# Kernel tuning notes

Measured on AMD Instinct MI355X. Metric: run time of the kernel, lower is better.

The kernel has to match this reference:

```python
import jax, jax.numpy as jnp
import numpy as np

N = 100000
E = 2000000
IN_DIM = 5
D = 32
L = 3
EPS = 1e-5


def setup_inputs() -> dict:
    key = jax.random.key(0)
    ks = jax.random.split(key, 10)
    x = jax.random.normal(ks[0], (N, IN_DIM), dtype=jnp.float32)
    edge_index = jax.random.randint(ks[1], (2, E), 0, N, dtype=jnp.int64)
    s = 1.0 / np.sqrt(D)
    w_in = jax.random.normal(ks[2], (D, IN_DIM), dtype=jnp.float32) / np.sqrt(IN_DIM)
    b_in = jnp.zeros((D,), dtype=jnp.float32)
    w_l = jax.random.normal(ks[3], (L, D, D), dtype=jnp.float32) * s  # lin_l per layer
    b_l = jnp.zeros((L, D), dtype=jnp.float32)
    w_r = jax.random.normal(ks[4], (L, D, D), dtype=jnp.float32) * s  # lin_r per layer (no bias, as in PyG SAGEConv)
    gamma = jnp.ones((D,), dtype=jnp.float32)
    beta = jnp.zeros((D,), dtype=jnp.float32)
    return {"x": x, "edge_index": edge_index, "w_in": w_in, "b_in": b_in,
            "w_l": w_l, "b_l": b_l, "w_r": w_r, "gamma": gamma, "beta": beta}


def _layernorm(h, gamma, beta):
    mu = jnp.mean(h, axis=-1, keepdims=True)
    var = jnp.mean(jnp.square(h - mu), axis=-1, keepdims=True)
    return (h - mu) * jax.lax.rsqrt(var + EPS) * gamma + beta


def reference(x, edge_index, w_in, b_in, w_l, b_l, w_r, gamma, beta):
    src = edge_index[0]
    dst = edge_index[1]
    n = x.shape[0]
    # node in-degree for mean aggregation (0-degree nodes get 0 output, like scatter_mean)
    deg = jax.ops.segment_sum(jnp.ones((src.shape[0],), dtype=x.dtype), dst, num_segments=n)
    inv_deg = (1.0 / jnp.maximum(deg, 1.0))[:, None]  # [N,1]
    h = x @ w_in.T + b_in  # [N, D]
    for i in range(w_l.shape[0]):
        msg = h[src]  # [E, D] gather
        agg = jax.ops.segment_sum(msg, dst, num_segments=n) * inv_deg  # mean aggregate
        h = agg @ w_l[i].T + b_l[i] + h @ w_r[i].T  # SAGEConv: lin_l(aggr) + lin_r(x)
        h = _layernorm(jax.nn.relu(h), gamma, beta)
    return h
```

## Files before the change

### kernel.cpp

```cpp
#include <hip/hip_runtime.h>
#include <hip/hip_bf16.h>

#define DIM 32
#define INDIM 5
#define EPB 4096
#define BKBITS 7
#define BKN 128
#define NBMAX 1024
#define CAP 4096

__device__ __forceinline__ unsigned short f2bf(float f) {
    unsigned u = __float_as_uint(f);
    u += 0x7FFFu + ((u >> 16) & 1u);
    return (unsigned short)(u >> 16);
}
__device__ __forceinline__ float bf2f_lo(unsigned u) { return __uint_as_float(u << 16); }
__device__ __forceinline__ float bf2f_hi(unsigned u) { return __uint_as_float(u & 0xFFFF0000u); }


__global__ __launch_bounds__(256) void bucket_count_kernel(const int* __restrict__ dst,
                                                           int* __restrict__ bcnt, int e, int nb) {
    __shared__ int hist[NBMAX];
    int t = threadIdx.x;
    for (int i = t; i < nb; i += 256) hist[i] = 0;
    __syncthreads();
    int base = blockIdx.x * EPB;
    for (int k = 0; k < EPB; k += 256) {
        int i = base + k + t;
        if (i < e) atomicAdd(&hist[dst[i] >> BKBITS], 1);
    }
    __syncthreads();
    for (int i = t; i < nb; i += 256) {
        int h = hist[i];
        if (h) atomicAdd(&bcnt[i], h);
    }
}


__global__ void bucket_scan_kernel(const int* __restrict__ bcnt, int* __restrict__ bbase,
                                   int* __restrict__ bcur, int* __restrict__ row_ptr,
                                   int nb, int n, int e) {
    __shared__ int s[1024];
    int t = threadIdx.x;
    int v = (t < nb) ? bcnt[t] : 0;
    s[t] = v;
    __syncthreads();
    for (int o = 1; o < 1024; o <<= 1) {
        int a = (t >= o) ? s[t - o] : 0;
        __syncthreads();
        s[t] += a;
        __syncthreads();
    }
    if (t < nb) {
        int excl = s[t] - v;
        bbase[t] = excl;
        bcur[t] = excl;
    }
    if (t == 0) {
        bbase[nb] = e;
        row_ptr[n] = e;
    }
}


__global__ __launch_bounds__(256) void bucket_fill_kernel(const int* __restrict__ src,
                                                          const int* __restrict__ dst,
                                                          int* __restrict__ bcur,
                                                          unsigned* __restrict__ packed,
                                                          int e, int nb) {
    __shared__ unsigned sw[EPB];
    __shared__ unsigned short sb[EPB];
    __shared__ int hist[NBMAX];
    __shared__ int rbase[NBMAX];
    int t = threadIdx.x;
    for (int i = t; i < nb; i += 256) hist[i] = 0;
    __syncthreads();
    int base = blockIdx.x * EPB;
    for (int k = 0; k < EPB; k += 256) {
        int i = base + k + t;
        if (i < e) {
            int s = src[i];
            int d = dst[i];
            int b = d >> BKBITS;
            sw[k + t] = ((unsigned)s << BKBITS) | (unsigned)(d & (BKN - 1));
            sb[k + t] = (unsigned short)b;
            atomicAdd(&hist[b], 1);
        }
    }
    __syncthreads();
    for (int i = t; i < nb; i += 256) {
        int h = hist[i];
        rbase[i] = h ? atomicAdd(&bcur[i], h) : 0;
        hist[i] = 0;
    }
    __syncthreads();
    for (int k = 0; k < EPB; k += 256) {
        int i = base + k + t;
        if (i < e) {
            int b = sb[k + t];
            int r = atomicAdd(&hist[b], 1);
            packed[rbase[b] + r] = sw[k + t];
        }
    }
}


__global__ __launch_bounds__(256) void csr_build_kernel(const unsigned* __restrict__ packed,
                                                        const int* __restrict__ bbase,
                                                        int* __restrict__ row_ptr,
                                                        int* __restrict__ esrc, int n) {
    __shared__ unsigned ew[CAP];
    __shared__ int h2[BKN];
    __shared__ int off[BKN];
    int b = blockIdx.x;
    int base = bbase[b];
    int cnt = bbase[b + 1] - base;
    int t = threadIdx.x;
    if (t < BKN) h2[t] = 0;
    __syncthreads();
    bool staged = (cnt <= CAP);
    for (int i = t; i < cnt; i += 256) {
        unsigned w = packed[base + i];
        if (staged) ew[i] = w;
        atomicAdd(&h2[w & (BKN - 1)], 1);
    }
    __syncthreads();
    int v = 0;
    if (t < BKN) {
        v = h2[t];
        off[t] = v;
    }
    __syncthreads();
    for (int o = 1; o < BKN; o <<= 1) {
        int a = 0;
        if (t < BKN && t >= o) a = off[t - o];
        __syncthreads();
        if (t < BKN) off[t] += a;
        __syncthreads();
    }
    if (t < BKN) {
        int excl = off[t] - v;
        __syncthreads();
        off[t] = excl;
        h2[t] = 0;
    } else {
        __syncthreads();
    }
    __syncthreads();
    int node = b * BKN + t;
    if (t < BKN && node < n) row_ptr[node] = base + off[t];
    for (int i = t; i < cnt; i += 256) {
        unsigned w = staged ? ew[i] : packed[base + i];
        int dl = w & (BKN - 1);
        int r = atomicAdd(&h2[dl], 1);
        esrc[base + off[dl] + r] = (int)(w >> BKBITS);
    }
}


__global__ void input_proj_kernel(const float* __restrict__ x, const float* __restrict__ w_in,
                                  const float* __restrict__ b_in,
                                  unsigned short* __restrict__ h, int n) {
    __shared__ float sw[DIM * INDIM];
    __shared__ float sb[DIM];
    int t = threadIdx.x;
    if (t < DIM * INDIM) sw[t] = w_in[t];
    if (t < DIM) sb[t] = b_in[t];
    __syncthreads();
    int idx = blockIdx.x * 256 + t;
    int node = idx >> 5;
    int d = idx & 31;
    if (node < n) {
        const float* xr = x + (size_t)node * INDIM;
        float acc = sb[d];
#pragma unroll
        for (int k = 0; k < INDIM; k++) acc = fmaf(xr[k], sw[d * INDIM + k], acc);
        h[(size_t)node * DIM + d] = f2bf(acc);
    }
}


template <int LAST>
__global__ __launch_bounds__(128, 4) void layer_fused_kernel(
    const int* __restrict__ row_ptr, const int* __restrict__ esrc,
    const unsigned short* __restrict__ h_in,
    unsigned short* __restrict__ h_out_bf, float* __restrict__ out_f32,
    const float* __restrict__ wl, const float* __restrict__ bl,
    const float* __restrict__ wr, const float* __restrict__ gamma,
    const float* __restrict__ beta, int n) {
    __shared__ float sAgg[32][DIM];
    __shared__ float sSelf[32][DIM];

    int t = threadIdx.x;
    int d = t & 31;

    int nd = t >> 2;
    int q = t & 3;
    int node = blockIdx.x * 32 + nd;
    const uint4* hv = (const uint4*)h_in;

    if (node < n) {
        {
            uint4 v = hv[(size_t)node * 4 + q];
            float4 f0 = make_float4(bf2f_lo(v.x), bf2f_hi(v.x), bf2f_lo(v.y), bf2f_hi(v.y));
            float4 f1 = make_float4(bf2f_lo(v.z), bf2f_hi(v.z), bf2f_lo(v.w), bf2f_hi(v.w));
            *(float4*)&sSelf[nd][q * 8] = f0;
            *(float4*)&sSelf[nd][q * 8 + 4] = f1;
        }
        int rs = row_ptr[node];
        int re = row_ptr[node + 1];
        float a0 = 0.f, a1 = 0.f, a2 = 0.f, a3 = 0.f, a4 = 0.f, a5 = 0.f, a6 = 0.f, a7 = 0.f;
        int j = rs;
        int i0, i1, i2, i3, i4, i5, i6, i7;
        bool have = (j + 8 <= re);
        if (have) {
            i0 = esrc[j];     i1 = esrc[j + 1]; i2 = esrc[j + 2]; i3 = esrc[j + 3];
            i4 = esrc[j + 4]; i5 = esrc[j + 5]; i6 = esrc[j + 6]; i7 = esrc[j + 7];
        }
        while (have) {
            int jn = j + 8;
            bool haven = (jn + 8 <= re);
            int t0, t1, t2, t3, t4, t5, t6, t7;
            if (haven) {
                t0 = esrc[jn];     t1 = esrc[jn + 1]; t2 = esrc[jn + 2]; t3 = esrc[jn + 3];
                t4 = esrc[jn + 4]; t5 = esrc[jn + 5]; t6 = esrc[jn + 6]; t7 = esrc[jn + 7];
            }
            uint4 v0 = hv[(size_t)i0 * 4 + q];
            uint4 v1 = hv[(size_t)i1 * 4 + q];
            uint4 v2 = hv[(size_t)i2 * 4 + q];
            uint4 v3 = hv[(size_t)i3 * 4 + q];
            uint4 v4 = hv[(size_t)i4 * 4 + q];
            uint4 v5 = hv[(size_t)i5 * 4 + q];
            uint4 v6 = hv[(size_t)i6 * 4 + q];
            uint4 v7 = hv[(size_t)i7 * 4 + q];
            a0 += bf2f_lo(v0.x); a1 += bf2f_hi(v0.x); a2 += bf2f_lo(v0.y); a3 += bf2f_hi(v0.y);
            a4 += bf2f_lo(v0.z); a5 += bf2f_hi(v0.z); a6 += bf2f_lo(v0.w); a7 += bf2f_hi(v0.w);
            a0 += bf2f_lo(v1.x); a1 += bf2f_hi(v1.x); a2 += bf2f_lo(v1.y); a3 += bf2f_hi(v1.y);
            a4 += bf2f_lo(v1.z); a5 += bf2f_hi(v1.z); a6 += bf2f_lo(v1.w); a7 += bf2f_hi(v1.w);
            a0 += bf2f_lo(v2.x); a1 += bf2f_hi(v2.x); a2 += bf2f_lo(v2.y); a3 += bf2f_hi(v2.y);
            a4 += bf2f_lo(v2.z); a5 += bf2f_hi(v2.z); a6 += bf2f_lo(v2.w); a7 += bf2f_hi(v2.w);
            a0 += bf2f_lo(v3.x); a1 += bf2f_hi(v3.x); a2 += bf2f_lo(v3.y); a3 += bf2f_hi(v3.y);
            a4 += bf2f_lo(v3.z); a5 += bf2f_hi(v3.z); a6 += bf2f_lo(v3.w); a7 += bf2f_hi(v3.w);
            a0 += bf2f_lo(v4.x); a1 += bf2f_hi(v4.x); a2 += bf2f_lo(v4.y); a3 += bf2f_hi(v4.y);
            a4 += bf2f_lo(v4.z); a5 += bf2f_hi(v4.z); a6 += bf2f_lo(v4.w); a7 += bf2f_hi(v4.w);
            a0 += bf2f_lo(v5.x); a1 += bf2f_hi(v5.x); a2 += bf2f_lo(v5.y); a3 += bf2f_hi(v5.y);
            a4 += bf2f_lo(v5.z); a5 += bf2f_hi(v5.z); a6 += bf2f_lo(v5.w); a7 += bf2f_hi(v5.w);
            a0 += bf2f_lo(v6.x); a1 += bf2f_hi(v6.x); a2 += bf2f_lo(v6.y); a3 += bf2f_hi(v6.y);
            a4 += bf2f_lo(v6.z); a5 += bf2f_hi(v6.z); a6 += bf2f_lo(v6.w); a7 += bf2f_hi(v6.w);
            a0 += bf2f_lo(v7.x); a1 += bf2f_hi(v7.x); a2 += bf2f_lo(v7.y); a3 += bf2f_hi(v7.y);
            a4 += bf2f_lo(v7.z); a5 += bf2f_hi(v7.z); a6 += bf2f_lo(v7.w); a7 += bf2f_hi(v7.w);
            j = jn;
            have = haven;
            if (haven) {
                i0 = t0; i1 = t1; i2 = t2; i3 = t3; i4 = t4; i5 = t5; i6 = t6; i7 = t7;
            }
        }
        for (; j < re; ++j) {
            int s = esrc[j];
            uint4 v = hv[(size_t)s * 4 + q];
            a0 += bf2f_lo(v.x); a1 += bf2f_hi(v.x); a2 += bf2f_lo(v.y); a3 += bf2f_hi(v.y);
            a4 += bf2f_lo(v.z); a5 += bf2f_hi(v.z); a6 += bf2f_lo(v.w); a7 += bf2f_hi(v.w);
        }
        float iv = 1.f / fmaxf((float)(re - rs), 1.f);
        float4 f0 = make_float4(a0 * iv, a1 * iv, a2 * iv, a3 * iv);
        float4 f1 = make_float4(a4 * iv, a5 * iv, a6 * iv, a7 * iv);
        *(float4*)&sAgg[nd][q * 8] = f0;
        *(float4*)&sAgg[nd][q * 8 + 4] = f1;
    }
    __syncthreads();

    float wlr[DIM], wrr[DIM];
    {
        const float4* p1 = (const float4*)(wl + (size_t)d * DIM);
        const float4* p2 = (const float4*)(wr + (size_t)d * DIM);
#pragma unroll
        for (int qq = 0; qq < 8; qq++) {
            float4 a = p1[qq];
            wlr[4 * qq] = a.x; wlr[4 * qq + 1] = a.y; wlr[4 * qq + 2] = a.z; wlr[4 * qq + 3] = a.w;
            float4 c = p2[qq];
            wrr[4 * qq] = c.x; wrr[4 * qq + 1] = c.y; wrr[4 * qq + 2] = c.z; wrr[4 * qq + 3] = c.w;
        }
    }
    float bias = bl[d], g = gamma[d], be = beta[d];

#pragma unroll
    for (int it = 0; it < 8; ++it) {
        int ln = it * 4 + (t >> 5);
        int nodec = blockIdx.x * 32 + ln;
        if (nodec < n) {
            float o = bias;
            const float* va = sAgg[ln];
            const float* vs = sSelf[ln];
#pragma unroll
            for (int qq = 0; qq < 8; qq++) {
                float4 a = *(const float4*)&va[qq * 4];
                float4 s = *(const float4*)&vs[qq * 4];
                o = fmaf(a.x, wlr[4 * qq], o);     o = fmaf(s.x, wrr[4 * qq], o);
                o = fmaf(a.y, wlr[4 * qq + 1], o); o = fmaf(s.y, wrr[4 * qq + 1], o);
                o = fmaf(a.z, wlr[4 * qq + 2], o); o = fmaf(s.z, wrr[4 * qq + 2], o);
                o = fmaf(a.w, wlr[4 * qq + 3], o); o = fmaf(s.w, wrr[4 * qq + 3], o);
            }
            float out = fmaxf(o, 0.f);
            float sum = out, sq = out * out;
#pragma unroll
            for (int off = 16; off > 0; off >>= 1) {
                sum += __shfl_xor(sum, off, 32);
                sq += __shfl_xor(sq, off, 32);
            }
            float mu = sum * (1.f / 32.f);
            float var = fmaxf(sq * (1.f / 32.f) - mu * mu, 0.f);
            float r = rsqrtf(var + 1e-5f);
            float res = (out - mu) * r * g + be;
            if (LAST) out_f32[(size_t)nodec * DIM + d] = res;
            else      h_out_bf[(size_t)nodec * DIM + d] = f2bf(res);
        }
    }
}


extern "C" void kernel_launch(void* const* d_in, const int* in_sizes, int n_in,
                              void* d_out, int out_size, void* d_ws, size_t ws_size,
                              hipStream_t stream) {
    const float* x = (const float*)d_in[0];
    const int* ei = (const int*)d_in[1];
    const float* w_in = (const float*)d_in[2];
    const float* b_in = (const float*)d_in[3];
    const float* w_l = (const float*)d_in[4];
    const float* b_l = (const float*)d_in[5];
    const float* w_r = (const float*)d_in[6];
    const float* gamma = (const float*)d_in[7];
    const float* beta = (const float*)d_in[8];

    int n = in_sizes[0] / INDIM;
    int e = in_sizes[1] / 2;
    int L = in_sizes[4] / (DIM * DIM);
    const int* src = ei;
    const int* dst = ei + e;
    int nb = (n + BKN - 1) >> BKBITS;

    char* w = (char*)d_ws;
    int* bcnt = (int*)w;               w += (size_t)NBMAX * 4;
    int* bbase = (int*)w;              w += (size_t)(NBMAX + 1) * 4;
    int* bcur = (int*)w;               w += (size_t)NBMAX * 4;
    int* row_ptr = (int*)w;            w += (size_t)(n + 1) * 4;
    int* esrc = (int*)w;               w += (size_t)e * 4;
    unsigned short* h_A = (unsigned short*)w;  w += (size_t)n * DIM * 2;
    unsigned short* h_B = (unsigned short*)w;  w += (size_t)n * DIM * 2;
    unsigned* packed = (unsigned*)h_A;

    int nbE = (e + EPB - 1) / EPB;

    hipMemsetAsync(bcnt, 0, (size_t)nb * 4, stream);
    bucket_count_kernel<<<nbE, 256, 0, stream>>>(dst, bcnt, e, nb);
    bucket_scan_kernel<<<1, 1024, 0, stream>>>(bcnt, bbase, bcur, row_ptr, nb, n, e);
    bucket_fill_kernel<<<nbE, 256, 0, stream>>>(src, dst, bcur, packed, e, nb);
    csr_build_kernel<<<nb, 256, 0, stream>>>(packed, bbase, row_ptr, esrc, n);

    input_proj_kernel<<<(n * DIM + 255) / 256, 256, 0, stream>>>(x, w_in, b_in, h_A, n);

    unsigned short* bufs[2] = {h_A, h_B};
    int nbF = (n + 31) / 32;
    for (int i = 0; i < L; i++) {
        const unsigned short* hin = bufs[i & 1];
        unsigned short* hout = bufs[(i + 1) & 1];
        const float* wl = w_l + (size_t)i * DIM * DIM;
        const float* bl = b_l + (size_t)i * DIM;
        const float* wr = w_r + (size_t)i * DIM * DIM;
        if (i == L - 1)
            layer_fused_kernel<1><<<nbF, 128, 0, stream>>>(row_ptr, esrc, hin, nullptr,
                                                           (float*)d_out, wl, bl, wr,
                                                           gamma, beta, n);
        else
            layer_fused_kernel<0><<<nbF, 128, 0, stream>>>(row_ptr, esrc, hin, hout,
                                                           nullptr, wl, bl, wr,
                                                           gamma, beta, n);
    }
}
```

Measured before the change: 242.2 us.

## Split bf16 node features into two half-planes and gather each plane separately

Stores the intermediate bf16 node features as two planes of 16 dims each (planar by half) instead of interleaved 32-dim rows. The aggregation now runs two passes, each gathering 32-byte half-rows, so each plane (3.2 MB) is more likely to stay resident in cache during its gather. The cost is walking each node's edge list twice and issuing narrower loads. It also adds nontemporal loads in the CSR build kernels and removes a redundant barrier.

```diff
diff --git a/kernel.cpp b/kernel.cpp
--- a/kernel.cpp
+++ b/kernel.cpp
@@ -27,7 +27,10 @@
     int base = blockIdx.x * EPB;
     for (int k = 0; k < EPB; k += 256) {
         int i = base + k + t;
-        if (i < e) atomicAdd(&hist[dst[i] >> BKBITS], 1);
+        if (i < e) {
+            int dv = __builtin_nontemporal_load(&dst[i]);
+            atomicAdd(&hist[dv >> BKBITS], 1);
+        }
     }
     __syncthreads();
     for (int i = t; i < nb; i += 256) {
@@ -79,8 +82,8 @@
     for (int k = 0; k < EPB; k += 256) {
         int i = base + k + t;
         if (i < e) {
-            int s = src[i];
-            int d = dst[i];
+            int s = __builtin_nontemporal_load(&src[i]);
+            int d = __builtin_nontemporal_load(&dst[i]);
             int b = d >> BKBITS;
             sw[k + t] = ((unsigned)s << BKBITS) | (unsigned)(d & (BKN - 1));
             sb[k + t] = (unsigned short)b;
@@ -120,7 +123,7 @@
     __syncthreads();
     bool staged = (cnt <= CAP);
     for (int i = t; i < cnt; i += 256) {
-        unsigned w = packed[base + i];
+        unsigned w = __builtin_nontemporal_load(&packed[base + i]);
         if (staged) ew[i] = w;
         atomicAdd(&h2[w & (BKN - 1)], 1);
     }
@@ -140,11 +143,8 @@
     }
     if (t < BKN) {
         int excl = off[t] - v;
-        __syncthreads();
         off[t] = excl;
         h2[t] = 0;
-    } else {
-        __syncthreads();
     }
     __syncthreads();
     int node = b * BKN + t;
@@ -175,7 +175,7 @@
         float acc = sb[d];
 #pragma unroll
         for (int k = 0; k < INDIM; k++) acc = fmaf(xr[k], sw[d * INDIM + k], acc);
-        h[(size_t)node * DIM + d] = f2bf(acc);
+        h[(size_t)(d >> 4) * n * 16 + (size_t)node * 16 + (d & 15)] = f2bf(acc);
     }
 }
 
@@ -193,79 +193,72 @@
 
     int t = threadIdx.x;
     int d = t & 31;
-
     int nd = t >> 2;
     int q = t & 3;
     int node = blockIdx.x * 32 + nd;
-    const uint4* hv = (const uint4*)h_in;
-
+
+    int rs = 0, re = 0;
     if (node < n) {
-        {
-            uint4 v = hv[(size_t)node * 4 + q];
-            float4 f0 = make_float4(bf2f_lo(v.x), bf2f_hi(v.x), bf2f_lo(v.y), bf2f_hi(v.y));
-            float4 f1 = make_float4(bf2f_lo(v.z), bf2f_hi(v.z), bf2f_lo(v.w), bf2f_hi(v.w));
-            *(float4*)&sSelf[nd][q * 8] = f0;
-            *(float4*)&sSelf[nd][q * 8 + 4] = f1;
-        }
-        int rs = row_ptr[node];
-        int re = row_ptr[node + 1];
-        float a0 = 0.f, a1 = 0.f, a2 = 0.f, a3 = 0.f, a4 = 0.f, a5 = 0.f, a6 = 0.f, a7 = 0.f;
-        int j = rs;
-        int i0, i1, i2, i3, i4, i5, i6, i7;
-        bool have = (j + 8 <= re);
-        if (have) {
-            i0 = esrc[j];     i1 = esrc[j + 1]; i2 = esrc[j + 2]; i3 = esrc[j + 3];
-            i4 = esrc[j + 4]; i5 = esrc[j + 5]; i6 = esrc[j + 6]; i7 = esrc[j + 7];
-        }
-        while (have) {
-            int jn = j + 8;
-            bool haven = (jn + 8 <= re);
-            int t0, t1, t2, t3, t4, t5, t6, t7;
-            if (haven) {
-                t0 = esrc[jn];     t1 = esrc[jn + 1]; t2 = esrc[jn + 2]; t3 = esrc[jn + 3];
-                t4 = esrc[jn + 4]; t5 = esrc[jn + 5]; t6 = esrc[jn + 6]; t7 = esrc[jn + 7];
-            }
-            uint4 v0 = hv[(size_t)i0 * 4 + q];
-            uint4 v1 = hv[(size_t)i1 * 4 + q];
-            uint4 v2 = hv[(size_t)i2 * 4 + q];
-            uint4 v3 = hv[(size_t)i3 * 4 + q];
-            uint4 v4 = hv[(size_t)i4 * 4 + q];
-            uint4 v5 = hv[(size_t)i5 * 4 + q];
-            uint4 v6 = hv[(size_t)i6 * 4 + q];
-            uint4 v7 = hv[(size_t)i7 * 4 + q];
-            a0 += bf2f_lo(v0.x); a1 += bf2f_hi(v0.x); a2 += bf2f_lo(v0.y); a3 += bf2f_hi(v0.y);
-            a4 += bf2f_lo(v0.z); a5 += bf2f_hi(v0.z); a6 += bf2f_lo(v0.w); a7 += bf2f_hi(v0.w);
-            a0 += bf2f_lo(v1.x); a1 += bf2f_hi(v1.x); a2 += bf2f_lo(v1.y); a3 += bf2f_hi(v1.y);
-            a4 += bf2f_lo(v1.z); a5 += bf2f_hi(v1.z); a6 += bf2f_lo(v1.w); a7 += bf2f_hi(v1.w);
-            a0 += bf2f_lo(v2.x); a1 += bf2f_hi(v2.x); a2 += bf2f_lo(v2.y); a3 += bf2f_hi(v2.y);
-            a4 += bf2f_lo(v2.z); a5 += bf2f_hi(v2.z); a6 += bf2f_lo(v2.w); a7 += bf2f_hi(v2.w);
-            a0 += bf2f_lo(v3.x); a1 += bf2f_hi(v3.x); a2 += bf2f_lo(v3.y); a3 += bf2f_hi(v3.y);
-            a4 += bf2f_lo(v3.z); a5 += bf2f_hi(v3.z); a6 += bf2f_lo(v3.w); a7 += bf2f_hi(v3.w);
-            a0 += bf2f_lo(v4.x); a1 += bf2f_hi(v4.x); a2 += bf2f_lo(v4.y); a3 += bf2f_hi(v4.y);
-            a4 += bf2f_lo(v4.z); a5 += bf2f_hi(v4.z); a6 += bf2f_lo(v4.w); a7 += bf2f_hi(v4.w);
-            a0 += bf2f_lo(v5.x); a1 += bf2f_hi(v5.x); a2 += bf2f_lo(v5.y); a3 += bf2f_hi(v5.y);
-            a4 += bf2f_lo(v5.z); a5 += bf2f_hi(v5.z); a6 += bf2f_lo(v5.w); a7 += bf2f_hi(v5.w);
-            a0 += bf2f_lo(v6.x); a1 += bf2f_hi(v6.x); a2 += bf2f_lo(v6.y); a3 += bf2f_hi(v6.y);
-            a4 += bf2f_lo(v6.z); a5 += bf2f_hi(v6.z); a6 += bf2f_lo(v6.w); a7 += bf2f_hi(v6.w);
-            a0 += bf2f_lo(v7.x); a1 += bf2f_hi(v7.x); a2 += bf2f_lo(v7.y); a3 += bf2f_hi(v7.y);
-            a4 += bf2f_lo(v7.z); a5 += bf2f_hi(v7.z); a6 += bf2f_lo(v7.w); a7 += bf2f_hi(v7.w);
-            j = jn;
-            have = haven;
-            if (haven) {
-                i0 = t0; i1 = t1; i2 = t2; i3 = t3; i4 = t4; i5 = t5; i6 = t6; i7 = t7;
-            }
-        }
-        for (; j < re; ++j) {
-            int s = esrc[j];
-            uint4 v = hv[(size_t)s * 4 + q];
-            a0 += bf2f_lo(v.x); a1 += bf2f_hi(v.x); a2 += bf2f_lo(v.y); a3 += bf2f_hi(v.y);
-            a4 += bf2f_lo(v.z); a5 += bf2f_hi(v.z); a6 += bf2f_lo(v.w); a7 += bf2f_hi(v.w);
-        }
-        float iv = 1.f / fmaxf((float)(re - rs), 1.f);
-        float4 f0 = make_float4(a0 * iv, a1 * iv, a2 * iv, a3 * iv);
-        float4 f1 = make_float4(a4 * iv, a5 * iv, a6 * iv, a7 * iv);
-        *(float4*)&sAgg[nd][q * 8] = f0;
-        *(float4*)&sAgg[nd][q * 8 + 4] = f1;
+        rs = row_ptr[node];
+        re = row_ptr[node + 1];
+    }
+    float iv = 1.f / fmaxf((float)(re - rs), 1.f);
+
+#pragma unroll
+    for (int p = 0; p < 2; ++p) {
+        const uint2* hv = (const uint2*)(h_in + (size_t)p * n * 16);
+        if (node < n) {
+            {
+                uint2 v = hv[(size_t)node * 4 + q];
+                float4 f = make_float4(bf2f_lo(v.x), bf2f_hi(v.x), bf2f_lo(v.y), bf2f_hi(v.y));
+                *(float4*)&sSelf[nd][p * 16 + q * 4] = f;
+            }
+            float a0 = 0.f, a1 = 0.f, a2 = 0.f, a3 = 0.f;
+            int j = rs;
+            int i0, i1, i2, i3, i4, i5, i6, i7;
+            bool have = (j + 8 <= re);
+            if (have) {
+                i0 = esrc[j];     i1 = esrc[j + 1]; i2 = esrc[j + 2]; i3 = esrc[j + 3];
+                i4 = esrc[j + 4]; i5 = esrc[j + 5]; i6 = esrc[j + 6]; i7 = esrc[j + 7];
+            }
+            while (have) {
+                int jn = j + 8;
+                bool haven = (jn + 8 <= re);
+                int t0, t1, t2, t3, t4, t5, t6, t7;
+                if (haven) {
+                    t0 = esrc[jn];     t1 = esrc[jn + 1]; t2 = esrc[jn + 2]; t3 = esrc[jn + 3];
+                    t4 = esrc[jn + 4]; t5 = esrc[jn + 5]; t6 = esrc[jn + 6]; t7 = esrc[jn + 7];
+                }
+                uint2 v0 = hv[(size_t)i0 * 4 + q];
+                uint2 v1 = hv[(size_t)i1 * 4 + q];
+                uint2 v2 = hv[(size_t)i2 * 4 + q];
+                uint2 v3 = hv[(size_t)i3 * 4 + q];
+                uint2 v4 = hv[(size_t)i4 * 4 + q];
+                uint2 v5 = hv[(size_t)i5 * 4 + q];
+                uint2 v6 = hv[(size_t)i6 * 4 + q];
+                uint2 v7 = hv[(size_t)i7 * 4 + q];
+                a0 += bf2f_lo(v0.x); a1 += bf2f_hi(v0.x); a2 += bf2f_lo(v0.y); a3 += bf2f_hi(v0.y);
+                a0 += bf2f_lo(v1.x); a1 += bf2f_hi(v1.x); a2 += bf2f_lo(v1.y); a3 += bf2f_hi(v1.y);
+                a0 += bf2f_lo(v2.x); a1 += bf2f_hi(v2.x); a2 += bf2f_lo(v2.y); a3 += bf2f_hi(v2.y);
+                a0 += bf2f_lo(v3.x); a1 += bf2f_hi(v3.x); a2 += bf2f_lo(v3.y); a3 += bf2f_hi(v3.y);
+                a0 += bf2f_lo(v4.x); a1 += bf2f_hi(v4.x); a2 += bf2f_lo(v4.y); a3 += bf2f_hi(v4.y);
+                a0 += bf2f_lo(v5.x); a1 += bf2f_hi(v5.x); a2 += bf2f_lo(v5.y); a3 += bf2f_hi(v5.y);
+                a0 += bf2f_lo(v6.x); a1 += bf2f_hi(v6.x); a2 += bf2f_lo(v6.y); a3 += bf2f_hi(v6.y);
+                a0 += bf2f_lo(v7.x); a1 += bf2f_hi(v7.x); a2 += bf2f_lo(v7.y); a3 += bf2f_hi(v7.y);
+                j = jn;
+                have = haven;
+                if (haven) {
+                    i0 = t0; i1 = t1; i2 = t2; i3 = t3; i4 = t4; i5 = t5; i6 = t6; i7 = t7;
+                }
+            }
+            for (; j < re; ++j) {
+                int s = esrc[j];
+                uint2 v = hv[(size_t)s * 4 + q];
+                a0 += bf2f_lo(v.x); a1 += bf2f_hi(v.x); a2 += bf2f_lo(v.y); a3 += bf2f_hi(v.y);
+            }
+            float4 f = make_float4(a0 * iv, a1 * iv, a2 * iv, a3 * iv);
+            *(float4*)&sAgg[nd][p * 16 + q * 4] = f;
+        }
     }
     __syncthreads();
 
@@ -312,7 +305,7 @@
             float r = rsqrtf(var + 1e-5f);
             float res = (out - mu) * r * g + be;
             if (LAST) out_f32[(size_t)nodec * DIM + d] = res;
-            else      h_out_bf[(size_t)nodec * DIM + d] = f2bf(res);
+            else      h_out_bf[(size_t)(d >> 4) * n * 16 + (size_t)nodec * 16 + (d & 15)] = f2bf(res);
         }
     }
 }
```

Result: slower. 273.7 us (+13.0%).
